# Kernel tuning notes

Measured on AMD Instinct MI355X. Metric: run time of the kernel, lower is better.

## Reference

```python
import jax, jax.numpy as jnp
import numpy as np
import math

TOKEN_DIM = 1024
NUM_HEADS = 16
HEAD_DIM = TOKEN_DIM // NUM_HEADS
T, B, N = 32, 32, 64


def setup_inputs() -> dict:
    key = jax.random.key(0)
    ks = jax.random.split(key, 9)
    query_vec = jax.random.normal(ks[0], (T, B, TOKEN_DIM), dtype=jnp.float32)
    tokens = jax.random.normal(ks[1], (T, B, N, TOKEN_DIM), dtype=jnp.float32)
    gate_logits = jax.random.normal(ks[2], (T, B, N), dtype=jnp.float32)
    scale = 1.0 / math.sqrt(TOKEN_DIM)
    Wq = jax.random.normal(ks[3], (TOKEN_DIM, TOKEN_DIM), dtype=jnp.float32) * scale
    Wk = jax.random.normal(ks[4], (TOKEN_DIM, TOKEN_DIM), dtype=jnp.float32) * scale
    Wv = jax.random.normal(ks[5], (TOKEN_DIM, TOKEN_DIM), dtype=jnp.float32) * scale
    bq = jnp.zeros((TOKEN_DIM,), dtype=jnp.float32)
    bk = jnp.zeros((TOKEN_DIM,), dtype=jnp.float32)
    bv = jnp.zeros((TOKEN_DIM,), dtype=jnp.float32)
    return {"query_vec": query_vec, "tokens": tokens, "gate_logits": gate_logits,
            "Wq": Wq, "bq": bq, "Wk": Wk, "bk": bk, "Wv": Wv, "bv": bv}


def reference(query_vec, tokens, gate_logits, Wq, bq, Wk, bk, Wv, bv):
    # QKV projections
    q = query_vec @ Wq + bq                      # [T,B,D]
    k = tokens @ Wk + bk                         # [T,B,N,D]
    v = tokens @ Wv + bv                         # [T,B,N,D]
    q = q.reshape(T, B, NUM_HEADS, HEAD_DIM)
    k = k.reshape(T, B, N, NUM_HEADS, HEAD_DIM)
    v = v.reshape(T, B, N, NUM_HEADS, HEAD_DIM)
    logits = jnp.einsum('tbhd,tbnhd->tbhn', q, k) / math.sqrt(HEAD_DIM)
    logits = logits + gate_logits[:, :, None, :]
    attn = jax.nn.softmax(logits, axis=-1)       # [T,B,H,N]
    attended = jnp.einsum('tbhn,tbnhd->tbhd', attn, v)
    attended = attended.reshape(T, B, TOKEN_DIM)
    mean_attn = attn.mean(axis=2)                # [T,B,N]
    return (attended, mean_attn, logits)
```

## Files before the change

### kernel.cpp

```cpp
#include <hip/hip_runtime.h>
#include <hip/hip_bf16.h>
#include <hip/hip_cooperative_groups.h>

namespace cg = cooperative_groups;

typedef __attribute__((ext_vector_type(4))) float f32x4;
typedef __attribute__((ext_vector_type(8))) short bf16x8;
typedef unsigned int u32;
typedef unsigned short u16;

#define DEV static __device__ __forceinline__


DEV u16 f2bf(float x){
  union { float f; u32 u; } v; v.f = x;
  u32 r = v.u + 0x7FFFu + ((v.u >> 16) & 1u);
  return (u16)(r >> 16);
}
DEV float bf2f(u16 s){
  union { u32 u; float f; } v; v.u = ((u32)s) << 16;
  return v.f;
}

#define MFMA16(a,b,c) __builtin_amdgcn_mfma_f32_16x16x32_bf16((a),(b),(c),0,0,0)

DEV int tok_off(int n, int dbyte){ return n*2048 + (dbyte ^ ((n & 7) << 4)); }

#define MEGA_DYN_LDS 65536

__global__ __launch_bounds__(256, 2) void k_mega(
    const float* __restrict__ qv, const float* __restrict__ tokens,
    const float* __restrict__ gate,
    const float* __restrict__ Wq, const float* __restrict__ bq,
    const float* __restrict__ Wk, const float* __restrict__ bk,
    const float* __restrict__ Wv, const float* __restrict__ bv,
    u16* __restrict__ qvB, u16* __restrict__ WqT, u16* __restrict__ WkB,
    u16* __restrict__ WvT, float* __restrict__ qf, u16* __restrict__ qb,
    u16* __restrict__ U, u16* __restrict__ ctxb,
    float* __restrict__ out_att, float* __restrict__ out_mean,
    float* __restrict__ out_logits){
  extern __shared__ __align__(16) char smem[];
  __shared__ __align__(16) char sstat[10496];
  cg::grid_group grid = cg::this_grid();
  const int tid = threadIdx.x;
  const int bx  = blockIdx.x;
  const int l = tid & 63, w = tid >> 6, g = l >> 4, li = l & 15;

  {
    const f32x4* s4 = (const f32x4*)qv;
    uint2* d2 = (uint2*)qvB;
    int g0 = bx*256 + tid;
    #pragma unroll
    for (int i = 0; i < 2; ++i){
      int idx = g0 + i*131072;
      f32x4 v = s4[idx];
      uint2 pk;
      pk.x = (u32)f2bf(v.x) | ((u32)f2bf(v.y) << 16);
      pk.y = (u32)f2bf(v.z) | ((u32)f2bf(v.w) << 16);
      d2[idx] = pk;
    }
  }
  {
    u16 (*tile)[65] = (u16 (*)[65])sstat;
    for (int tl = bx; tl < 768; tl += 512){
      __syncthreads();
      const int which = tl >> 8, t8 = tl & 255;
      const float* src = which==0 ? Wq : (which==1 ? Wk : Wv);
      const int bi = (t8 >> 4) << 6, bj = (t8 & 15) << 6;
      #pragma unroll
      for (int k2 = 0; k2 < 16; ++k2){
        int e = tid + (k2 << 8); int r = e >> 6, c = e & 63;
        tile[r][c] = f2bf(src[(size_t)(bi + r)*1024 + bj + c]);
      }
      __syncthreads();
      if (which == 1){
        #pragma unroll
        for (int k2 = 0; k2 < 16; ++k2){
          int e = tid + (k2 << 8); int r = e >> 6, c = e & 63;
          WkB[(size_t)(bi + r)*1024 + bj + c] = tile[r][c];
        }
      } else {
        u16* dst = which==0 ? WqT : WvT;
        #pragma unroll
        for (int k2 = 0; k2 < 16; ++k2){
          int e = tid + (k2 << 8); int r = e >> 6, c = e & 63;
          dst[(size_t)(bj + r)*1024 + bi + c] = tile[c][r];
        }
      }
    }
  }
  __threadfence(); grid.sync(); __threadfence();

  {
    const int wm = w & 1, wn = w >> 1;
    const int m_base = (bx >> 5)*64 + wm*32;
    const int n_base = (bx & 31)*32 + wn*16;
    f32x4 acc[2]; acc[0] = (f32x4)0.0f; acc[1] = (f32x4)0.0f;
    #pragma unroll 4
    for (int kb = 0; kb < 32; ++kb){
      const int k0 = kb*32 + g*8;
      bf16x8 b = *(const bf16x8*)(WqT + (size_t)(n_base + li)*1024 + k0);
      #pragma unroll
      for (int rt = 0; rt < 2; ++rt){
        bf16x8 a = *(const bf16x8*)(qvB + (size_t)(m_base + rt*16 + li)*1024 + k0);
        acc[rt] = MFMA16(a, b, acc[rt]);
      }
    }
    #pragma unroll
    for (int rt = 0; rt < 2; ++rt)
      #pragma unroll
      for (int r = 0; r < 4; ++r){
        int m = m_base + rt*16 + g*4 + r;
        int n = n_base + li;
        float val = acc[rt][r] + bq[n];
        qf[(size_t)m*1024 + n] = val;
        qb[(size_t)m*1024 + n] = f2bf(val);
      }
  }
  __threadfence(); grid.sync(); __threadfence();

  {
    u16 (*stile)[64] = (u16 (*)[64])sstat;
    const int wm = w & 1, wn = w >> 1;
    for (int i = 0; i < 8; ++i){
      const int tl = bx*8 + i;
      const int tb0 = (tl >> 8)*64, d0 = ((tl >> 4) & 15)*64, h = tl & 15;
      f32x4 acc[2][2];
      #pragma unroll
      for (int a0=0;a0<2;++a0)
        #pragma unroll
        for (int b0=0;b0<2;++b0) acc[a0][b0] = (f32x4)0.0f;
      #pragma unroll
      for (int kb = 0; kb < 2; ++kb){
        const int k0 = h*64 + kb*32 + g*8;
        bf16x8 a[2], b[2];
        #pragma unroll
        for (int rt=0;rt<2;++rt)
          a[rt] = *(const bf16x8*)(qb + (size_t)(tb0 + wm*32 + rt*16 + li)*1024 + k0);
        #pragma unroll
        for (int ct=0;ct<2;++ct)
          b[ct] = *(const bf16x8*)(WkB + (size_t)(d0 + wn*32 + ct*16 + li)*1024 + k0);
        #pragma unroll
        for (int rt=0;rt<2;++rt)
          #pragma unroll
          for (int ct=0;ct<2;++ct)
            acc[rt][ct] = MFMA16(a[rt], b[ct], acc[rt][ct]);
      }
      __syncthreads();
      #pragma unroll
      for (int rt=0;rt<2;++rt)
        #pragma unroll
        for (int ct=0;ct<2;++ct)
          #pragma unroll
          for (int r=0;r<4;++r)
            stile[wm*32 + rt*16 + g*4 + r][wn*32 + ct*16 + li] = f2bf(acc[rt][ct][r]);
      __syncthreads();
      const int rr = tid >> 2, cg4 = tid & 3;
      f32x4* dst = (f32x4*)(U + ((size_t)(tb0 + rr)*16 + h)*1024 + d0 + cg4*16);
      const f32x4* s4 = (const f32x4*)(&stile[rr][cg4*16]);
      dst[0] = s4[0]; dst[1] = s4[1];
    }
  }
  __threadfence(); grid.sync(); __threadfence();

  {
    float* part_s   = (float*)(sstat);
    float* logits_s = (float*)(sstat + 4096);
    float* p_s      = (float*)(sstat + 8192);
    float* csum     = (float*)(sstat + 10240);
    float* r_s      = (float*)(sstat + 10304);
    float* mzs      = (float*)(sstat + 10368);
    const int sh = tid >> 4, sj = tid & 15;

    __syncthreads();

    {
      const f32x4* src4 = (const f32x4*)(tokens + (size_t)bx*65536);
      f32x4 pstg[16];
      #pragma unroll
      for (int it = 0; it < 16; ++it) pstg[it] = src4[(size_t)it*256 + tid];
      #pragma unroll
      for (int it = 0; it < 16; ++it){
        f32x4 v = pstg[it];
        uint2 pk;
        pk.x = (u32)f2bf(v.x) | ((u32)f2bf(v.y) << 16);
        pk.y = (u32)f2bf(v.z) | ((u32)f2bf(v.w) << 16);
        *(uint2*)(smem + tok_off(it, tid*8)) = pk;
      }
    }

    float m_run = -1e30f, z_run = 0.0f;
    f32x4 cacc[4][4];
    bf16x8 a[8];

    for (int r = 0; r < 8; ++r){
      const int c = r & 3, n0 = c*16;
      const int tb = bx + (r >> 2)*512;
      char* bufc = smem + (size_t)(r & 1)*32768;

      f32x4 stg[16];
      const int rn = r + 1;
      if (rn < 8){
        const f32x4* srcn = (const f32x4*)(tokens
            + (size_t)(bx + (rn >> 2)*512)*65536 + (size_t)((rn & 3)*16)*1024);
        #pragma unroll
        for (int it = 0; it < 16; ++it)
          stg[it] = srcn[(size_t)it*256 + tid];
        __builtin_amdgcn_sched_barrier(0);
      }
      __builtin_amdgcn_sched_barrier(0);

      if (c == 0){
        m_run = -1e30f; z_run = 0.0f;
        #pragma unroll
        for (int i=0;i<4;++i)
          #pragma unroll
          for (int j=0;j<4;++j) cacc[i][j] = (f32x4)0.0f;
        const bf16x8* Ub = (const bf16x8*)(U + (size_t)tb*16384);
        #pragma unroll
        for (int i = 0; i < 8; ++i)
          a[i] = Ub[li*128 + (w*8 + i)*4 + g];
        const float* qp = qf + (size_t)tb*1024 + sh*64 + sj*4;
        const float* bp = bk + sh*64 + sj*4;
        float part = qp[0]*bp[0] + qp[1]*bp[1] + qp[2]*bp[2] + qp[3]*bp[3];
        part += __shfl_xor(part, 1); part += __shfl_xor(part, 2);
        part += __shfl_xor(part, 4); part += __shfl_xor(part, 8);
        if (sj == 0) csum[sh] = part;
      }

      __syncthreads();

      {
        f32x4 acc = (f32x4)0.0f;
        #pragma unroll
        for (int i = 0; i < 8; ++i){
          bf16x8 b = *(const bf16x8*)(bufc + tok_off(li, ((w*8 + i)*32 + g*8)*2));
          acc = MFMA16(a[i], b, acc);
        }
        *(f32x4*)(part_s + (size_t)(w*64 + l)*4) = acc;
        __syncthreads();
        if (w == 0){
          acc += *(const f32x4*)(part_s + (size_t)(64  + l)*4);
          acc += *(const f32x4*)(part_s + (size_t)(128 + l)*4);
          acc += *(const f32x4*)(part_s + (size_t)(192 + l)*4);
          float gv = gate[(size_t)tb*64 + n0 + li];
          #pragma unroll
          for (int rg = 0; rg < 4; ++rg){
            int h = g*4 + rg;
            logits_s[h*64 + n0 + li] = (acc[rg] + csum[h])*0.125f + gv;
          }
        }
        __syncthreads();
      }

      {
        float lv = logits_s[sh*64 + n0 + sj];
        out_logits[(size_t)tb*1024 + sh*64 + n0 + sj] = lv;
        float cm = lv;
        cm = fmaxf(cm, __shfl_xor(cm, 1)); cm = fmaxf(cm, __shfl_xor(cm, 2));
        cm = fmaxf(cm, __shfl_xor(cm, 4)); cm = fmaxf(cm, __shfl_xor(cm, 8));
        float m_new = fmaxf(m_run, cm);
        float rsc = __expf(m_run - m_new);
        float p0 = __expf(lv - m_new);
        float zs = p0;
        zs += __shfl_xor(zs, 1); zs += __shfl_xor(zs, 2);
        zs += __shfl_xor(zs, 4); zs += __shfl_xor(zs, 8);
        z_run = z_run * rsc + zs;
        m_run = m_new;
        p_s[sj*16 + sh] = p0;
        if (sj == 0){
          r_s[sh] = rsc;
          if (c == 3){ mzs[sh*2] = m_new; mzs[sh*2 + 1] = 1.0f / z_run; }
        }
      }
      __syncthreads();

      {
        float rr4[4];
        #pragma unroll
        for (int hh = 0; hh < 4; ++hh) rr4[hh] = r_s[w*4 + hh];
        #pragma unroll
        for (int dq = 0; dq < 4; ++dq)
          #pragma unroll
          for (int hh = 0; hh < 4; ++hh) cacc[dq][hh] *= rr4[hh];
        for (int nl = 0; nl < 16; ++nl){
          f32x4 p = *(const f32x4*)(p_s + nl*16 + w*4);
          #pragma unroll
          for (int dq = 0; dq < 4; ++dq){
            uint2 t2 = *(const uint2*)(bufc + tok_off(nl, (dq*256 + l*4)*2));
            float f0 = bf2f((u16)(t2.x & 0xFFFFu));
            float f1 = bf2f((u16)(t2.x >> 16));
            float f2 = bf2f((u16)(t2.y & 0xFFFFu));
            float f3 = bf2f((u16)(t2.y >> 16));
            #pragma unroll
            for (int hh = 0; hh < 4; ++hh){
              float av = p[hh];
              cacc[dq][hh].x += av*f0; cacc[dq][hh].y += av*f1;
              cacc[dq][hh].z += av*f2; cacc[dq][hh].w += av*f3;
            }
          }
        }
      }

      if (rn < 8){
        char* bufn = smem + (size_t)(rn & 1)*32768;
        #pragma unroll
        for (int it = 0; it < 16; ++it){
          f32x4 v = stg[it];
          uint2 pk;
          pk.x = (u32)f2bf(v.x) | ((u32)f2bf(v.y) << 16);
          pk.y = (u32)f2bf(v.z) | ((u32)f2bf(v.w) << 16);
          *(uint2*)(bufn + tok_off(it, tid*8)) = pk;
        }
      }

      if (c == 3){
        if (tid < 64){
          float s = 0.0f;
          #pragma unroll
          for (int h = 0; h < 16; ++h)
            s += __expf(logits_s[h*64 + tid] - mzs[h*2]) * mzs[h*2 + 1];
          out_mean[(size_t)tb*64 + tid] = s * 0.0625f;
        }
        #pragma unroll
        for (int hh = 0; hh < 4; ++hh){
          const int h = w*4 + hh;
          const float zinv = mzs[h*2 + 1];
          #pragma unroll
          for (int dq = 0; dq < 4; ++dq){
            f32x4 v = cacc[dq][hh];
            uint2 pk;
            pk.x = (u32)f2bf(v.x * zinv) | ((u32)f2bf(v.y * zinv) << 16);
            pk.y = (u32)f2bf(v.z * zinv) | ((u32)f2bf(v.w * zinv) << 16);
            *(uint2*)(ctxb + ((size_t)tb*16 + h)*1024 + dq*256 + l*4) = pk;
          }
        }
      }
    }
  }
  __threadfence(); grid.sync(); __threadfence();

  {
    const int wm = w & 1, wn = w >> 1;
    const int m_base = (bx >> 4)*32, h = bx & 15;
    f32x4 acc[2]; acc[0] = (f32x4)0.0f; acc[1] = (f32x4)0.0f;
    #pragma unroll 4
    for (int kb = 0; kb < 32; ++kb){
      const int k0 = kb*32 + g*8;
      bf16x8 a = *(const bf16x8*)(ctxb + ((size_t)(m_base + wm*16 + li)*16 + h)*1024 + k0);
      #pragma unroll
      for (int ct = 0; ct < 2; ++ct){
        bf16x8 b = *(const bf16x8*)(WvT + (size_t)(h*64 + wn*32 + ct*16 + li)*1024 + k0);
        acc[ct] = MFMA16(a, b, acc[ct]);
      }
    }
    #pragma unroll
    for (int ct = 0; ct < 2; ++ct)
      #pragma unroll
      for (int r = 0; r < 4; ++r){
        int m = m_base + wm*16 + g*4 + r;
        int dout = h*64 + wn*32 + ct*16 + li;
        out_att[(size_t)m*1024 + dout] = acc[ct][r] + bv[dout];
      }
  }
}

__global__ __launch_bounds__(256) void k_convert(
    const float* __restrict__ Wq, const float* __restrict__ Wk, const float* __restrict__ Wv,
    u16* __restrict__ WqT, u16* __restrict__ WkB, u16* __restrict__ WvT){
  __shared__ u16 tile[64][65];
  const int which = blockIdx.y;
  const float* src = which==0 ? Wq : (which==1 ? Wk : Wv);
  const int bi = (blockIdx.x >> 4) << 6;
  const int bj = (blockIdx.x & 15) << 6;
  const int t  = threadIdx.x;
  #pragma unroll
  for (int k2 = 0; k2 < 16; ++k2){
    int e = t + (k2 << 8);
    int r = e >> 6, c = e & 63;
    tile[r][c] = f2bf(src[(size_t)(bi + r)*1024 + bj + c]);
  }
  __syncthreads();
  if (which == 1){
    #pragma unroll
    for (int k2 = 0; k2 < 16; ++k2){
      int e = t + (k2 << 8); int r = e >> 6, c = e & 63;
      WkB[(size_t)(bi + r)*1024 + bj + c] = tile[r][c];
    }
  } else {
    u16* dst = which==0 ? WqT : WvT;
    #pragma unroll
    for (int k2 = 0; k2 < 16; ++k2){
      int e = t + (k2 << 8); int r = e >> 6, c = e & 63;
      dst[(size_t)(bj + r)*1024 + bi + c] = tile[c][r];
    }
  }
}

__global__ __launch_bounds__(256) void k_qproj(
    const float* __restrict__ qv, const u16* __restrict__ WqT, const float* __restrict__ bq,
    float* __restrict__ qf, u16* __restrict__ qb){
  const int l = threadIdx.x & 63, w = threadIdx.x >> 6;
  const int wm = w & 1, wn = w >> 1;
  const int g = l >> 4, li = l & 15;
  const int m_base = blockIdx.x*64 + wm*32;
  const int n_base = blockIdx.y*64 + wn*32;
  f32x4 acc[2][2];
  #pragma unroll
  for (int i=0;i<2;++i)
    #pragma unroll
    for (int j=0;j<2;++j) acc[i][j] = (f32x4)0.0f;

  #pragma unroll 4
  for (int kb = 0; kb < 32; ++kb){
    const int k0 = kb*32 + g*8;
    bf16x8 a[2], b[2];
    #pragma unroll
    for (int rt = 0; rt < 2; ++rt){
      const float* p = qv + (size_t)(m_base + rt*16 + li)*1024 + k0;
      f32x4 lo = *(const f32x4*)p;
      f32x4 hi = *(const f32x4*)(p+4);
      union { u16 s[8]; bf16x8 v; } u;
      u.s[0]=f2bf(lo.x); u.s[1]=f2bf(lo.y); u.s[2]=f2bf(lo.z); u.s[3]=f2bf(lo.w);
      u.s[4]=f2bf(hi.x); u.s[5]=f2bf(hi.y); u.s[6]=f2bf(hi.z); u.s[7]=f2bf(hi.w);
      a[rt] = u.v;
    }
    #pragma unroll
    for (int ct = 0; ct < 2; ++ct)
      b[ct] = *(const bf16x8*)(WqT + (size_t)(n_base + ct*16 + li)*1024 + k0);
    #pragma unroll
    for (int rt = 0; rt < 2; ++rt)
      #pragma unroll
      for (int ct = 0; ct < 2; ++ct)
        acc[rt][ct] = MFMA16(a[rt], b[ct], acc[rt][ct]);
  }
  #pragma unroll
  for (int rt=0;rt<2;++rt)
    #pragma unroll
    for (int ct=0;ct<2;++ct)
      #pragma unroll
      for (int r=0;r<4;++r){
        int m = m_base + rt*16 + g*4 + r;
        int n = n_base + ct*16 + li;
        float val = acc[rt][ct][r] + bq[n];
        qf[(size_t)m*1024 + n] = val;
        qb[(size_t)m*1024 + n] = f2bf(val);
      }
}

__global__ __launch_bounds__(256) void k_umat(
    const u16* __restrict__ qb, const u16* __restrict__ WkB, u16* __restrict__ U){
  __shared__ __align__(16) u16 stile[64][64];
  const int l = threadIdx.x & 63, w = threadIdx.x >> 6;
  const int wm = w & 1, wn = w >> 1, g = l >> 4, li = l & 15;
  const int tb0 = blockIdx.x*64, d0 = blockIdx.y*64, h = blockIdx.z;
  f32x4 acc[2][2];
  #pragma unroll
  for (int i=0;i<2;++i)
    #pragma unroll
    for (int j=0;j<2;++j) acc[i][j] = (f32x4)0.0f;

  #pragma unroll
  for (int kb = 0; kb < 2; ++kb){
    const int k0 = h*64 + kb*32 + g*8;
    bf16x8 a[2], b[2];
    #pragma unroll
    for (int rt=0;rt<2;++rt)
      a[rt] = *(const bf16x8*)(qb + (size_t)(tb0 + wm*32 + rt*16 + li)*1024 + k0);
    #pragma unroll
    for (int ct=0;ct<2;++ct)
      b[ct] = *(const bf16x8*)(WkB + (size_t)(d0 + wn*32 + ct*16 + li)*1024 + k0);
    #pragma unroll
    for (int rt=0;rt<2;++rt)
      #pragma unroll
      for (int ct=0;ct<2;++ct)
        acc[rt][ct] = MFMA16(a[rt], b[ct], acc[rt][ct]);
  }
  #pragma unroll
  for (int rt=0;rt<2;++rt)
    #pragma unroll
    for (int ct=0;ct<2;++ct)
      #pragma unroll
      for (int r=0;r<4;++r)
        stile[wm*32 + rt*16 + g*4 + r][wn*32 + ct*16 + li] = f2bf(acc[rt][ct][r]);
  __syncthreads();
  const int r = threadIdx.x >> 2, cg4 = threadIdx.x & 3;
  f32x4* dst = (f32x4*)(U + ((size_t)(tb0 + r)*16 + h)*1024 + d0 + cg4*16);
  const f32x4* s4 = (const f32x4*)(&stile[r][cg4*16]);
  dst[0] = s4[0]; dst[1] = s4[1];
}

#define K3_LDS 76032
__global__ __launch_bounds__(256, 2) void k_attn(
    const float* __restrict__ tokens, const float* __restrict__ gate,
    const u16* __restrict__ U, const float* __restrict__ qf, const float* __restrict__ bk,
    float* __restrict__ out_logits, float* __restrict__ out_mean, u16* __restrict__ ctx){
  extern __shared__ __align__(16) char smem[];
  float* part_s   = (float*)(smem + 65536);
  float* logits_s = (float*)(smem + 69632);
  float* p_s      = (float*)(smem + 73728);
  float* csum     = (float*)(smem + 75776);
  float* r_s      = (float*)(smem + 75840);
  float* mzs      = (float*)(smem + 75904);
  const int tb = blockIdx.x;
  const int tid = threadIdx.x;
  const int l = tid & 63, w = tid >> 6, g = l >> 4, li = l & 15;
  const int nt = w & 1, kh = w >> 1;
  const int sh = tid >> 4, sj = tid & 15;

  bf16x8 a[16];
  const bf16x8* Ub = (const bf16x8*)(U + (size_t)tb*16384);
  #pragma unroll
  for (int i = 0; i < 16; ++i)
    a[i] = Ub[li*128 + (kh*16 + i)*4 + g];

  {
    const float* qp = qf + (size_t)tb*1024 + sh*64 + sj*4;
    const float* bp = bk + sh*64 + sj*4;
    float part = qp[0]*bp[0] + qp[1]*bp[1] + qp[2]*bp[2] + qp[3]*bp[3];
    part += __shfl_xor(part, 1); part += __shfl_xor(part, 2);
    part += __shfl_xor(part, 4); part += __shfl_xor(part, 8);
    if (sj == 0) csum[sh] = part;
  }

  float m_run = -1e30f, z_run = 0.0f;
  f32x4 cacc[4][4];
  #pragma unroll
  for (int i=0;i<4;++i)
    #pragma unroll
    for (int j=0;j<4;++j) cacc[i][j] = (f32x4)0.0f;

  const f32x4* src4 = (const f32x4*)(tokens + (size_t)tb*65536);

  for (int c = 0; c < 2; ++c){
    const int n0 = c*32;
    __syncthreads();
    #pragma unroll 8
    for (int it = 0; it < 32; ++it){
      f32x4 v = src4[(size_t)(n0 + it)*256 + tid];
      uint2 pk;
      pk.x = (u32)f2bf(v.x) | ((u32)f2bf(v.y) << 16);
      pk.y = (u32)f2bf(v.z) | ((u32)f2bf(v.w) << 16);
      *(uint2*)(smem + tok_off(it, tid*8)) = pk;
    }
    __syncthreads();
    {
      f32x4 acc = (f32x4)0.0f;
      #pragma unroll
      for (int i = 0; i < 16; ++i){
        int kb = kh*16 + i;
        bf16x8 b = *(const bf16x8*)(smem + tok_off(nt*16 + li, (kb*32 + g*8)*2));
        acc = MFMA16(a[i], b, acc);
      }
      *(f32x4*)(part_s + (size_t)(w*64 + l)*4) = acc;
      __syncthreads();
      if (kh == 0){
        acc += *(const f32x4*)(part_s + (size_t)((w+2)*64 + l)*4);
        float gv = gate[(size_t)tb*64 + n0 + nt*16 + li];
        #pragma unroll
        for (int r = 0; r < 4; ++r){
          int h = g*4 + r;
          logits_s[h*64 + n0 + nt*16 + li] = (acc[r] + csum[h])*0.125f + gv;
        }
      }
      __syncthreads();
    }
    {
      float lv0 = logits_s[sh*64 + n0 + sj];
      float lv1 = logits_s[sh*64 + n0 + 16 + sj];
      out_logits[(size_t)tb*1024 + sh*64 + n0 + sj]      = lv0;
      out_logits[(size_t)tb*1024 + sh*64 + n0 + 16 + sj] = lv1;
      float cm = fmaxf(lv0, lv1);
      cm = fmaxf(cm, __shfl_xor(cm, 1)); cm = fmaxf(cm, __shfl_xor(cm, 2));
      cm = fmaxf(cm, __shfl_xor(cm, 4)); cm = fmaxf(cm, __shfl_xor(cm, 8));
      float m_new = fmaxf(m_run, cm);
      float rsc = __expf(m_run - m_new);
      float p0 = __expf(lv0 - m_new), p1 = __expf(lv1 - m_new);
      float zs = p0 + p1;
      zs += __shfl_xor(zs, 1); zs += __shfl_xor(zs, 2);
      zs += __shfl_xor(zs, 4); zs += __shfl_xor(zs, 8);
      z_run = z_run * rsc + zs;
      m_run = m_new;
      p_s[sj*16 + sh]        = p0;
      p_s[(sj + 16)*16 + sh] = p1;
      if (sj == 0){
        r_s[sh] = rsc;
        if (c == 1){ mzs[sh*2] = m_new; mzs[sh*2 + 1] = 1.0f / z_run; }
      }
    }
    __syncthreads();
    {
      float rr[4];
      #pragma unroll
      for (int hh = 0; hh < 4; ++hh) rr[hh] = r_s[w*4 + hh];
      #pragma unroll
      for (int dq = 0; dq < 4; ++dq)
        #pragma unroll
        for (int hh = 0; hh < 4; ++hh) cacc[dq][hh] *= rr[hh];
      for (int nl = 0; nl < 32; ++nl){
        f32x4 p = *(const f32x4*)(p_s + nl*16 + w*4);
        #pragma unroll
        for (int dq = 0; dq < 4; ++dq){
          uint2 t2 = *(const uint2*)(smem + tok_off(nl, (dq*256 + l*4)*2));
          float f0 = bf2f((u16)(t2.x & 0xFFFFu));
          float f1 = bf2f((u16)(t2.x >> 16));
          float f2 = bf2f((u16)(t2.y & 0xFFFFu));
          float f3 = bf2f((u16)(t2.y >> 16));
          #pragma unroll
          for (int hh = 0; hh < 4; ++hh){
            float av = p[hh];
            cacc[dq][hh].x += av*f0; cacc[dq][hh].y += av*f1;
            cacc[dq][hh].z += av*f2; cacc[dq][hh].w += av*f3;
          }
        }
      }
    }
  }

  if (tid < 64){
    float s = 0.0f;
    #pragma unroll
    for (int h = 0; h < 16; ++h)
      s += __expf(logits_s[h*64 + tid] - mzs[h*2]) * mzs[h*2 + 1];
    out_mean[(size_t)tb*64 + tid] = s * 0.0625f;
  }

  #pragma unroll
  for (int hh = 0; hh < 4; ++hh){
    const int h = w*4 + hh;
    const float zinv = mzs[h*2 + 1];
    #pragma unroll
    for (int dq = 0; dq < 4; ++dq){
      f32x4 v = cacc[dq][hh];
      uint2 pk;
      pk.x = (u32)f2bf(v.x * zinv) | ((u32)f2bf(v.y * zinv) << 16);
      pk.y = (u32)f2bf(v.z * zinv) | ((u32)f2bf(v.w * zinv) << 16);
      *(uint2*)(ctx + ((size_t)tb*16 + h)*1024 + dq*256 + l*4) = pk;
    }
  }
}

__global__ __launch_bounds__(256) void k_attended(
    const u16* __restrict__ ctx, const u16* __restrict__ WvT, const float* __restrict__ bv,
    float* __restrict__ out_att){
  const int l = threadIdx.x & 63, w = threadIdx.x >> 6;
  const int wm = w & 1, wn = w >> 1, g = l >> 4, li = l & 15;
  const int tb0 = blockIdx.x*64, h = blockIdx.y;
  f32x4 acc[2][2];
  #pragma unroll
  for (int i=0;i<2;++i)
    #pragma unroll
    for (int j=0;j<2;++j) acc[i][j] = (f32x4)0.0f;

  #pragma unroll 4
  for (int kb = 0; kb < 32; ++kb){
    const int k0 = kb*32 + g*8;
    bf16x8 a[2], b[2];
    #pragma unroll
    for (int rt=0;rt<2;++rt)
      a[rt] = *(const bf16x8*)(ctx + ((size_t)(tb0 + wm*32 + rt*16 + li)*16 + h)*1024 + k0);
    #pragma unroll
    for (int ct=0;ct<2;++ct)
      b[ct] = *(const bf16x8*)(WvT + (size_t)(h*64 + wn*32 + ct*16 + li)*1024 + k0);
    #pragma unroll
    for (int rt=0;rt<2;++rt)
      #pragma unroll
      for (int ct=0;ct<2;++ct)
        acc[rt][ct] = MFMA16(a[rt], b[ct], acc[rt][ct]);
  }
  #pragma unroll
  for (int rt=0;rt<2;++rt)
    #pragma unroll
    for (int ct=0;ct<2;++ct)
      #pragma unroll
      for (int r=0;r<4;++r){
        int m = tb0 + wm*32 + rt*16 + g*4 + r;
        int dout = h*64 + wn*32 + ct*16 + li;
        out_att[(size_t)m*1024 + dout] = acc[rt][ct][r] + bv[dout];
      }
}

extern "C" void kernel_launch(void* const* d_in, const int* in_sizes, int n_in,
                              void* d_out, int out_size, void* d_ws, size_t ws_size,
                              hipStream_t stream){
  const float* qv     = (const float*)d_in[0];
  const float* tokens = (const float*)d_in[1];
  const float* gate   = (const float*)d_in[2];
  const float* Wq     = (const float*)d_in[3];
  const float* bq     = (const float*)d_in[4];
  const float* Wk     = (const float*)d_in[5];
  const float* bk     = (const float*)d_in[6];
  const float* Wv     = (const float*)d_in[7];
  const float* bv     = (const float*)d_in[8];

  char* ws = (char*)d_ws;
  u16*   qvB = (u16*)(ws);
  u16*   WqT = (u16*)(ws + (2u<<20));
  u16*   WkB = (u16*)(ws + (4u<<20));
  u16*   WvT = (u16*)(ws + (6u<<20));
  float* qf  = (float*)(ws + (8u<<20));
  u16*   qb  = (u16*)(ws + (12u<<20));
  u16*   U   = (u16*)(ws + (14u<<20));
  u16*   ctxb= (u16*)(ws + (46u<<20));

  float* out_att    = (float*)d_out;
  float* out_mean   = out_att + 1048576;
  float* out_logits = out_att + 1114112;

  int dev = 0; (void)hipGetDevice(&dev);
  int coop = 0; (void)hipDeviceGetAttribute(&coop, hipDeviceAttributeCooperativeLaunch, dev);
  int ncu = 0;  (void)hipDeviceGetAttribute(&ncu, hipDeviceAttributeMultiprocessorCount, dev);
  int perCU = 0;
  hipError_t oe = hipOccupancyMaxActiveBlocksPerMultiprocessor(
                      &perCU, (const void*)k_mega, 256, (size_t)MEGA_DYN_LDS);
  bool use_coop = (coop != 0) && (oe == hipSuccess) && ((long)perCU * (long)ncu >= 512);

  if (use_coop){
    void* args[] = { (void*)&qv, (void*)&tokens, (void*)&gate,
                     (void*)&Wq, (void*)&bq, (void*)&Wk, (void*)&bk,
                     (void*)&Wv, (void*)&bv,
                     (void*)&qvB, (void*)&WqT, (void*)&WkB, (void*)&WvT,
                     (void*)&qf, (void*)&qb, (void*)&U, (void*)&ctxb,
                     (void*)&out_att, (void*)&out_mean, (void*)&out_logits };
    hipError_t le = hipLaunchCooperativeKernel((const void*)k_mega, dim3(512), dim3(256),
                                               args, MEGA_DYN_LDS, stream);
    if (le == hipSuccess) return;
    use_coop = false;
  }

  (void)hipFuncSetAttribute((const void*)k_attn,
                            hipFuncAttributeMaxDynamicSharedMemorySize, K3_LDS);
  k_convert <<<dim3(256, 3),    256, 0,      stream>>>(Wq, Wk, Wv, WqT, WkB, WvT);
  k_qproj   <<<dim3(16, 16),    256, 0,      stream>>>(qv, WqT, bq, qf, qb);
  k_umat    <<<dim3(16, 16, 16),256, 0,      stream>>>(qb, WkB, U);
  k_attn    <<<dim3(1024),      256, K3_LDS, stream>>>(tokens, gate, U, qf, bk,
                                                       out_logits, out_mean, ctxb);
  k_attended<<<dim3(16, 16),    256, 0,      stream>>>(ctxb, WvT, bv, out_att);
}
```

Before: 177.4 us.

## Stage fp32 tokens directly into LDS via global_load_lds with 8-token chunks

Replaces the register-staged fp32→bf16 conversion of token tiles with direct global-to-LDS async loads of raw fp32 data, swizzled, in 8-token chunks (16 rounds instead of 8). Conversion to bf16 now happens at MFMA operand load time with packed cvt instructions, and the PV accumulation reads fp32 directly. The logit reduction is restructured so all threads sum partials after a lightweight barrier, removing a serialized wave-0 step. This trades more rounds and barriers, plus double the LDS bytes per token, for freeing registers and overlapping loads asynchronously.

Result: no change. 177.3 us (-0.1%).

```diff
diff --git a/kernel.cpp b/kernel.cpp
--- a/kernel.cpp
+++ b/kernel.cpp
@@ -25,6 +25,39 @@
 #define MFMA16(a,b,c) __builtin_amdgcn_mfma_f32_16x16x32_bf16((a),(b),(c),0,0,0)
 
 DEV int tok_off(int n, int dbyte){ return n*2048 + (dbyte ^ ((n & 7) << 4)); }
+
+#define SWZ(n) ((((n)&3)<<5) | ((((n)>>2)&1)<<4))
+
+DEV void bar_lgkm(){
+  __builtin_amdgcn_sched_barrier(0);
+  asm volatile("s_waitcnt lgkmcnt(0)" ::: "memory");
+  __builtin_amdgcn_s_barrier();
+  __builtin_amdgcn_sched_barrier(0);
+}
+
+DEV bf16x8 cvt8(f32x4 lo, f32x4 hi){
+  union { u32 u[4]; bf16x8 v; } r;
+  asm("v_cvt_pk_bf16_f32 %0, %1, %2" : "=v"(r.u[0]) : "v"(lo.x), "v"(lo.y));
+  asm("v_cvt_pk_bf16_f32 %0, %1, %2" : "=v"(r.u[1]) : "v"(lo.z), "v"(lo.w));
+  asm("v_cvt_pk_bf16_f32 %0, %1, %2" : "=v"(r.u[2]) : "v"(hi.x), "v"(hi.y));
+  asm("v_cvt_pk_bf16_f32 %0, %1, %2" : "=v"(r.u[3]) : "v"(hi.z), "v"(hi.w));
+  return r.v;
+}
+
+DEV void stage8(const float* __restrict__ tokens, int tbn, int tk0,
+                char* smem, int bb, int w, int l){
+  char* ldsb = smem + (size_t)bb*32768 + (size_t)w*8192;
+  const char* gb = (const char*)tokens + (size_t)tbn*262144 + (size_t)tk0*4096;
+  #pragma unroll
+  for (int j = 0; j < 8; ++j){
+    const int nloc  = w*2 + (j >> 2);
+    const int inner = (((j & 3)*1024) + l*16) ^ SWZ(nloc);
+    __builtin_amdgcn_global_load_lds(
+        (const __attribute__((address_space(1))) u32*)(gb + (size_t)nloc*4096 + inner),
+        (__attribute__((address_space(3))) u32*)(ldsb + j*1024),
+        16, 0, 0);
+  }
+}
 
 #define MEGA_DYN_LDS 65536
 
@@ -173,42 +206,20 @@
     const int sh = tid >> 4, sj = tid & 15;
 
     __syncthreads();
-
-    {
-      const f32x4* src4 = (const f32x4*)(tokens + (size_t)bx*65536);
-      f32x4 pstg[16];
-      #pragma unroll
-      for (int it = 0; it < 16; ++it) pstg[it] = src4[(size_t)it*256 + tid];
-      #pragma unroll
-      for (int it = 0; it < 16; ++it){
-        f32x4 v = pstg[it];
-        uint2 pk;
-        pk.x = (u32)f2bf(v.x) | ((u32)f2bf(v.y) << 16);
-        pk.y = (u32)f2bf(v.z) | ((u32)f2bf(v.w) << 16);
-        *(uint2*)(smem + tok_off(it, tid*8)) = pk;
-      }
-    }
+    stage8(tokens, bx, 0, smem, 0, w, l);
 
     float m_run = -1e30f, z_run = 0.0f;
     f32x4 cacc[4][4];
     bf16x8 a[8];
 
-    for (int r = 0; r < 8; ++r){
-      const int c = r & 3, n0 = c*16;
-      const int tb = bx + (r >> 2)*512;
+    for (int r = 0; r < 16; ++r){
+      const int c = r & 7, n0 = c*8;
+      const int tb = bx + (r >> 3)*512;
       char* bufc = smem + (size_t)(r & 1)*32768;
 
-      f32x4 stg[16];
-      const int rn = r + 1;
-      if (rn < 8){
-        const f32x4* srcn = (const f32x4*)(tokens
-            + (size_t)(bx + (rn >> 2)*512)*65536 + (size_t)((rn & 3)*16)*1024);
-        #pragma unroll
-        for (int it = 0; it < 16; ++it)
-          stg[it] = srcn[(size_t)it*256 + tid];
-        __builtin_amdgcn_sched_barrier(0);
-      }
-      __builtin_amdgcn_sched_barrier(0);
+      __syncthreads();
+      if (r + 1 < 16)
+        stage8(tokens, bx + ((r+1) >> 3)*512, ((r+1) & 7)*8, smem, (r+1) & 1, w, l);
 
       if (c == 0){
         m_run = -1e30f; z_run = 0.0f;
@@ -228,52 +239,45 @@
         if (sj == 0) csum[sh] = part;
       }
 
-      __syncthreads();
-
       {
+        const int row = li & 7;
+        const int sw  = SWZ(row);
         f32x4 acc = (f32x4)0.0f;
         #pragma unroll
         for (int i = 0; i < 8; ++i){
-          bf16x8 b = *(const bf16x8*)(bufc + tok_off(li, ((w*8 + i)*32 + g*8)*2));
-          acc = MFMA16(a[i], b, acc);
+          const int p0b = (w*8 + i)*128 + g*32;
+          f32x4 lo = *(const f32x4*)(bufc + row*4096 + ((p0b     ) ^ sw));
+          f32x4 hi = *(const f32x4*)(bufc + row*4096 + ((p0b + 16) ^ sw));
+          acc = MFMA16(a[i], cvt8(lo, hi), acc);
         }
         *(f32x4*)(part_s + (size_t)(w*64 + l)*4) = acc;
-        __syncthreads();
-        if (w == 0){
-          acc += *(const f32x4*)(part_s + (size_t)(64  + l)*4);
-          acc += *(const f32x4*)(part_s + (size_t)(128 + l)*4);
-          acc += *(const f32x4*)(part_s + (size_t)(192 + l)*4);
-          float gv = gate[(size_t)tb*64 + n0 + li];
-          #pragma unroll
-          for (int rg = 0; rg < 4; ++rg){
-            int h = g*4 + rg;
-            logits_s[h*64 + n0 + li] = (acc[rg] + csum[h])*0.125f + gv;
-          }
-        }
-        __syncthreads();
-      }
-
-      {
-        float lv = logits_s[sh*64 + n0 + sj];
+      }
+      bar_lgkm();
+
+      if (sj < 8){
+        const int idx = ((sh >> 2)*16 + sj)*4 + (sh & 3);
+        float lv = part_s[idx] + part_s[256 + idx] + part_s[512 + idx] + part_s[768 + idx];
+        lv = (lv + csum[sh])*0.125f + gate[(size_t)tb*64 + n0 + sj];
+        logits_s[sh*64 + n0 + sj] = lv;
         out_logits[(size_t)tb*1024 + sh*64 + n0 + sj] = lv;
         float cm = lv;
-        cm = fmaxf(cm, __shfl_xor(cm, 1)); cm = fmaxf(cm, __shfl_xor(cm, 2));
-        cm = fmaxf(cm, __shfl_xor(cm, 4)); cm = fmaxf(cm, __shfl_xor(cm, 8));
+        cm = fmaxf(cm, __shfl_xor(cm, 1));
+        cm = fmaxf(cm, __shfl_xor(cm, 2));
+        cm = fmaxf(cm, __shfl_xor(cm, 4));
         float m_new = fmaxf(m_run, cm);
         float rsc = __expf(m_run - m_new);
         float p0 = __expf(lv - m_new);
         float zs = p0;
-        zs += __shfl_xor(zs, 1); zs += __shfl_xor(zs, 2);
-        zs += __shfl_xor(zs, 4); zs += __shfl_xor(zs, 8);
+        zs += __shfl_xor(zs, 1); zs += __shfl_xor(zs, 2); zs += __shfl_xor(zs, 4);
         z_run = z_run * rsc + zs;
         m_run = m_new;
         p_s[sj*16 + sh] = p0;
         if (sj == 0){
           r_s[sh] = rsc;
-          if (c == 3){ mzs[sh*2] = m_new; mzs[sh*2 + 1] = 1.0f / z_run; }
-        }
-      }
-      __syncthreads();
+          if (c == 7){ mzs[sh*2] = m_new; mzs[sh*2 + 1] = 1.0f / z_run; }
+        }
+      }
+      bar_lgkm();
 
       {
         float rr4[4];
@@ -283,38 +287,21 @@
         for (int dq = 0; dq < 4; ++dq)
           #pragma unroll
           for (int hh = 0; hh < 4; ++hh) cacc[dq][hh] *= rr4[hh];
-        for (int nl = 0; nl < 16; ++nl){
-          f32x4 p = *(const f32x4*)(p_s + nl*16 + w*4);
+        #pragma unroll
+        for (int nl = 0; nl < 8; ++nl){
+          const f32x4 p = *(const f32x4*)(p_s + nl*16 + w*4);
+          const int swn = SWZ(nl);
           #pragma unroll
           for (int dq = 0; dq < 4; ++dq){
-            uint2 t2 = *(const uint2*)(bufc + tok_off(nl, (dq*256 + l*4)*2));
-            float f0 = bf2f((u16)(t2.x & 0xFFFFu));
-            float f1 = bf2f((u16)(t2.x >> 16));
-            float f2 = bf2f((u16)(t2.y & 0xFFFFu));
-            float f3 = bf2f((u16)(t2.y >> 16));
+            const f32x4 t = *(const f32x4*)(bufc + (size_t)nl*4096 + ((dq*1024 + l*16) ^ swn));
             #pragma unroll
-            for (int hh = 0; hh < 4; ++hh){
-              float av = p[hh];
-              cacc[dq][hh].x += av*f0; cacc[dq][hh].y += av*f1;
-              cacc[dq][hh].z += av*f2; cacc[dq][hh].w += av*f3;
-            }
+            for (int hh = 0; hh < 4; ++hh)
+              cacc[dq][hh] += t * p[hh];
           }
         }
       }
 
-      if (rn < 8){
-        char* bufn = smem + (size_t)(rn & 1)*32768;
-        #pragma unroll
-        for (int it = 0; it < 16; ++it){
-          f32x4 v = stg[it];
-          uint2 pk;
-          pk.x = (u32)f2bf(v.x) | ((u32)f2bf(v.y) << 16);
-          pk.y = (u32)f2bf(v.z) | ((u32)f2bf(v.w) << 16);
-          *(uint2*)(bufn + tok_off(it, tid*8)) = pk;
-        }
-      }
-
-      if (c == 3){
+      if (c == 7){
         if (tid < 64){
           float s = 0.0f;
           #pragma unroll
```
